# Optimization experiments

Hardware: AMD Instinct MI355X
Metric: run time of the kernel (lower is better)

The kernel has to match this reference:

```python
import jax, jax.numpy as jnp
import numpy as np

N = 100000      # nodes
E = 1600000     # edges (avg degree 16)
IN = 128        # input_dim
H = 8           # heads
D = 8           # hidden_dim (== heads, required by the diversity-loss bmm)
HD = H * D      # per-layer width
OUT = 10        # output_dim
G = 64          # graphs in batch
NEG = 0.2       # GATConv leaky_relu slope
DIVW = 0.1      # diversity_weight


def setup_inputs() -> dict:
    key = jax.random.key(0)
    ks = jax.random.split(key, 20)
    w = lambda k, shape, fan: (jax.random.normal(k, shape, jnp.float32) / np.sqrt(fan)).astype(jnp.float32)
    inp = {}
    inp['x'] = jax.random.normal(ks[0], (N, IN), jnp.float32)
    inp['edge_index'] = jax.random.randint(ks[1], (2, E), 0, N, dtype=jnp.int32)
    inp['batch'] = jnp.sort(jax.random.randint(ks[2], (N,), 0, G, dtype=jnp.int32))
    # layer 0: GATConv(IN -> D, heads=H)
    inp['W0'] = w(ks[3], (IN, HD), IN)
    inp['att_src0'] = w(ks[4], (H, D), D)
    inp['att_dst0'] = w(ks[5], (H, D), D)
    inp['b0'] = jnp.zeros((HD,), jnp.float32)
    inp['gamma0'] = jnp.ones((HD,), jnp.float32)
    inp['beta0'] = jnp.zeros((HD,), jnp.float32)
    inp['P0'] = w(ks[6], (H, D), D)
    # layer 1: GATConv(HD -> D, heads=H)
    inp['W1'] = w(ks[7], (HD, HD), HD)
    inp['att_src1'] = w(ks[8], (H, D), D)
    inp['att_dst1'] = w(ks[9], (H, D), D)
    inp['b1'] = jnp.zeros((HD,), jnp.float32)
    inp['gamma1'] = jnp.ones((HD,), jnp.float32)
    inp['beta1'] = jnp.zeros((HD,), jnp.float32)
    inp['P1'] = w(ks[10], (H, D), D)
    inp['fc_W'] = w(ks[11], (HD, OUT), HD)
    inp['fc_b'] = jnp.zeros((OUT,), jnp.float32)
    return inp


def _gat(x, src, dst, W, a_src, a_dst, b):
    h = (x @ W).reshape(-1, H, D)                       # [N,H,D]
    al = jnp.sum(h * a_src, -1)                          # [N,H] src scores
    ar = jnp.sum(h * a_dst, -1)                          # [N,H] dst scores
    e = jax.nn.leaky_relu(al[src] + ar[dst], NEG)        # [E,H]
    m = jax.ops.segment_max(e, dst, num_segments=N)      # per-dst max (stable softmax)
    m = jnp.where(jnp.isfinite(m), m, 0.0)
    ex = jnp.exp(e - m[dst])
    den = jax.ops.segment_sum(ex, dst, num_segments=N)
    a = ex / (den[dst] + 1e-16)                          # PyG softmax eps
    out = jax.ops.segment_sum(a[:, :, None] * h[src], dst, num_segments=N)  # [N,H,D]
    return out.reshape(-1, HD) + b


def _bn(x, g, b):  # BatchNorm1d, training-mode batch stats, eps=1e-5
    mu = x.mean(0)
    var = x.var(0)
    return g * (x - mu) * jax.lax.rsqrt(var + 1e-5) + b


def _div_loss(x, P):
    xr = x.reshape(-1, H, D)
    pr = jnp.einsum('nij,jk->nik', xr, P)                # bmm with shared projector (needs D==H)
    nh = pr / jnp.maximum(jnp.linalg.norm(pr, axis=-1, keepdims=True), 1e-8)
    S = jnp.einsum('nid,njd->ij', nh, nh) / x.shape[0]   # mean-over-nodes cosine sims [H,H]
    iu = jnp.triu_indices(H, 1)
    return jnp.mean(S[iu] ** 2)


def reference(x, edge_index, batch, W0, att_src0, att_dst0, b0, gamma0, beta0, P0,
              W1, att_src1, att_dst1, b1, gamma1, beta1, P1, fc_W, fc_b):
    src, dst = edge_index[0], edge_index[1]
    dl = 0.0
    h = _gat(x, src, dst, W0, att_src0, att_dst0, b0)
    dl = dl + _div_loss(h, P0)
    h = jax.nn.elu(_bn(h, gamma0, beta0))
    h = _gat(h, src, dst, W1, att_src1, att_dst1, b1)
    dl = dl + _div_loss(h, P1)
    h = jax.nn.elu(_bn(h, gamma1, beta1))
    cnt = jax.ops.segment_sum(jnp.ones((N,), h.dtype), batch, num_segments=G)
    pooled = jax.ops.segment_sum(h, batch, num_segments=G) / jnp.maximum(cnt, 1.0)[:, None]
    logits = pooled @ fc_W + fc_b
    return logits, DIVW * dl
```

## Files before the change

kernel.cpp:

```cpp
#include <hip/hip_runtime.h>
#include <hip/hip_fp16.h>

#define NB 100000
#define NE 1600000
#define PSH 12500
#define BCAP 64

typedef int iv4 __attribute__((ext_vector_type(4)));

__device__ __forceinline__ float elu_f(float x) { return x > 0.f ? x : expm1f(x); }

__global__ __launch_bounds__(256) void k_fill_zero(float4* __restrict__ p, int n4) {
    int i = blockIdx.x * 256 + threadIdx.x, s = gridDim.x * 256;
    float4 z = make_float4(0.f, 0.f, 0.f, 0.f);
    for (; i < n4; i += s) p[i] = z;
}

__global__ __launch_bounds__(256) void k_scatter(const iv4* __restrict__ src4, const iv4* __restrict__ dst4,
                                                 int* __restrict__ cnt, int* __restrict__ buck, int ne4) {
    int part = blockIdx.x & 7;
    unsigned lo = part * PSH;
    int pb = blockIdx.x >> 3, npb = gridDim.x >> 3;
    int i = pb * 256 + threadIdx.x, st = npb * 256;
    for (; i < ne4; i += st) {
        iv4 d = dst4[i];
        bool bx = (unsigned)(d.x - lo) < PSH;
        bool by = (unsigned)(d.y - lo) < PSH;
        bool bz = (unsigned)(d.z - lo) < PSH;
        bool bw = (unsigned)(d.w - lo) < PSH;
        if (!(bx | by | bz | bw)) continue;
        iv4 s = src4[i];
        if (bx) buck[(d.x << 6) + (atomicAdd(&cnt[d.x], 1) & (BCAP - 1))] = s.x;
        if (by) buck[(d.y << 6) + (atomicAdd(&cnt[d.y], 1) & (BCAP - 1))] = s.y;
        if (bz) buck[(d.z << 6) + (atomicAdd(&cnt[d.z], 1) & (BCAP - 1))] = s.z;
        if (bw) buck[(d.w << 6) + (atomicAdd(&cnt[d.w], 1) & (BCAP - 1))] = s.w;
    }
}

template<int K, bool BN>
__global__ __launch_bounds__(256) void k_gemm(
    const float* __restrict__ X, const float* __restrict__ W,
    const float* __restrict__ attS, const float* __restrict__ attD,
    const float* __restrict__ bscale, const float* __restrict__ bshift,
    __half* __restrict__ Hout, float* __restrict__ al, float* __restrict__ ar, int nrows)
{
    constexpr int NC = K / 64;
    __shared__ float4 xs4[64][16];
    __shared__ float  ws_[64][64];
    int t = threadIdx.x;
    int rowBase = blockIdx.x * 64;
    int r = t & 63, cg = t >> 6, c0 = cg * 16;
    float acc[16];
#pragma unroll
    for (int j = 0; j < 16; ++j) acc[j] = 0.f;
    int sw = r & 15;

    for (int kc = 0; kc < NC; ++kc) {
        if (kc) __syncthreads();
        for (int i = t; i < 1024; i += 256)
            ((float4*)ws_)[i] = ((const float4*)W)[kc * 1024 + i];
        for (int i = t; i < 1024; i += 256) {
            int rr = i >> 4, c4 = i & 15;
            int gr = rowBase + rr;
            float4 v = make_float4(0.f, 0.f, 0.f, 0.f);
            if (gr < nrows) v = ((const float4*)X)[gr * (K / 4) + kc * 16 + c4];
            if (BN) {
                int c = (kc * 16 + c4) * 4;
                v.x = elu_f(bscale[c + 0] * v.x + bshift[c + 0]);
                v.y = elu_f(bscale[c + 1] * v.y + bshift[c + 1]);
                v.z = elu_f(bscale[c + 2] * v.z + bshift[c + 2]);
                v.w = elu_f(bscale[c + 3] * v.w + bshift[c + 3]);
            }
            xs4[rr][c4 ^ (rr & 15)] = v;
        }
        __syncthreads();

        for (int k4 = 0; k4 < 16; ++k4) {
            float4 xv = xs4[r][k4 ^ sw];
            float xk[4] = {xv.x, xv.y, xv.z, xv.w};
#pragma unroll
            for (int kk = 0; kk < 4; ++kk) {
                const float* wrow = &ws_[k4 * 4 + kk][c0];
                float4 wa = *(const float4*)(wrow + 0);
                float4 wb = *(const float4*)(wrow + 4);
                float4 wc = *(const float4*)(wrow + 8);
                float4 wd = *(const float4*)(wrow + 12);
                float x = xk[kk];
                acc[0]  += x * wa.x; acc[1]  += x * wa.y; acc[2]  += x * wa.z; acc[3]  += x * wa.w;
                acc[4]  += x * wb.x; acc[5]  += x * wb.y; acc[6]  += x * wb.z; acc[7]  += x * wb.w;
                acc[8]  += x * wc.x; acc[9]  += x * wc.y; acc[10] += x * wc.z; acc[11] += x * wc.w;
                acc[12] += x * wd.x; acc[13] += x * wd.y; acc[14] += x * wd.z; acc[15] += x * wd.w;
            }
        }
    }

    int gr = rowBase + r;
    if (gr < nrows) {
        __half2 hp[8];
#pragma unroll
        for (int j = 0; j < 8; ++j) hp[j] = __floats2half2_rn(acc[2 * j], acc[2 * j + 1]);
        uint4* op = (uint4*)(Hout + (size_t)gr * 64 + c0);
        op[0] = *(uint4*)&hp[0];
        op[1] = *(uint4*)&hp[4];
#pragma unroll
        for (int hh = 0; hh < 2; ++hh) {
            int h = cg * 2 + hh;
            float sa = 0.f, sd = 0.f;
#pragma unroll
            for (int d = 0; d < 8; ++d) {
                float hv = acc[hh * 8 + d];
                sa += hv * attS[h * 8 + d];
                sd += hv * attD[h * 8 + d];
            }
            al[gr * 8 + h] = sa;
            ar[gr * 8 + h] = sd;
        }
    }
}

__global__ __launch_bounds__(256) void k_agg(const int* __restrict__ cnt, const int* __restrict__ buck,
    const float* __restrict__ al, const float* __restrict__ ar,
    const __half* __restrict__ Hf, const float* __restrict__ bias,
    float* __restrict__ agg, int n)
{
    int lane = threadIdx.x & 63;
    int w  = __builtin_amdgcn_readfirstlane((blockIdx.x * 256 + (int)threadIdx.x) >> 6);
    int nw = (gridDim.x * 256) >> 6;
    int h = lane >> 3;
    float bl = bias[lane];
    for (int d = w; d < n; d += nw) {
        int r0 = d << 6;
        int r1 = r0 + __builtin_amdgcn_readfirstlane(cnt[d]);
        float arh = ar[d * 8 + h];
        float ac0 = 0.f, ac1 = 0.f, ac2 = 0.f, ac3 = 0.f, ac4 = 0.f, ac5 = 0.f, ac6 = 0.f, ac7 = 0.f;
        float de0 = 0.f, de1 = 0.f, de2 = 0.f, de3 = 0.f, de4 = 0.f, de5 = 0.f, de6 = 0.f, de7 = 0.f;
        int p = r0;
        for (; p + 8 <= r1; p += 8) {
            int s0 = __builtin_amdgcn_readfirstlane(buck[p]);
            int s1 = __builtin_amdgcn_readfirstlane(buck[p + 1]);
            int s2 = __builtin_amdgcn_readfirstlane(buck[p + 2]);
            int s3 = __builtin_amdgcn_readfirstlane(buck[p + 3]);
            int s4 = __builtin_amdgcn_readfirstlane(buck[p + 4]);
            int s5 = __builtin_amdgcn_readfirstlane(buck[p + 5]);
            int s6 = __builtin_amdgcn_readfirstlane(buck[p + 6]);
            int s7 = __builtin_amdgcn_readfirstlane(buck[p + 7]);
            float t0 = al[s0 * 8 + h] + arh;
            float t1 = al[s1 * 8 + h] + arh;
            float t2 = al[s2 * 8 + h] + arh;
            float t3 = al[s3 * 8 + h] + arh;
            float t4 = al[s4 * 8 + h] + arh;
            float t5 = al[s5 * 8 + h] + arh;
            float t6 = al[s6 * 8 + h] + arh;
            float t7 = al[s7 * 8 + h] + arh;
            float h0 = __half2float(Hf[((size_t)s0 << 6) + lane]);
            float h1 = __half2float(Hf[((size_t)s1 << 6) + lane]);
            float h2 = __half2float(Hf[((size_t)s2 << 6) + lane]);
            float h3 = __half2float(Hf[((size_t)s3 << 6) + lane]);
            float h4 = __half2float(Hf[((size_t)s4 << 6) + lane]);
            float h5 = __half2float(Hf[((size_t)s5 << 6) + lane]);
            float h6 = __half2float(Hf[((size_t)s6 << 6) + lane]);
            float h7 = __half2float(Hf[((size_t)s7 << 6) + lane]);
            t0 = t0 > 0.f ? t0 : 0.2f * t0;  t1 = t1 > 0.f ? t1 : 0.2f * t1;
            t2 = t2 > 0.f ? t2 : 0.2f * t2;  t3 = t3 > 0.f ? t3 : 0.2f * t3;
            t4 = t4 > 0.f ? t4 : 0.2f * t4;  t5 = t5 > 0.f ? t5 : 0.2f * t5;
            t6 = t6 > 0.f ? t6 : 0.2f * t6;  t7 = t7 > 0.f ? t7 : 0.2f * t7;
            float e0 = __expf(t0), e1 = __expf(t1), e2 = __expf(t2), e3 = __expf(t3);
            float e4 = __expf(t4), e5 = __expf(t5), e6 = __expf(t6), e7 = __expf(t7);
            de0 += e0; ac0 = fmaf(e0, h0, ac0);
            de1 += e1; ac1 = fmaf(e1, h1, ac1);
            de2 += e2; ac2 = fmaf(e2, h2, ac2);
            de3 += e3; ac3 = fmaf(e3, h3, ac3);
            de4 += e4; ac4 = fmaf(e4, h4, ac4);
            de5 += e5; ac5 = fmaf(e5, h5, ac5);
            de6 += e6; ac6 = fmaf(e6, h6, ac6);
            de7 += e7; ac7 = fmaf(e7, h7, ac7);
        }
        for (; p + 4 <= r1; p += 4) {
            int s0 = __builtin_amdgcn_readfirstlane(buck[p]);
            int s1 = __builtin_amdgcn_readfirstlane(buck[p + 1]);
            int s2 = __builtin_amdgcn_readfirstlane(buck[p + 2]);
            int s3 = __builtin_amdgcn_readfirstlane(buck[p + 3]);
            float t0 = al[s0 * 8 + h] + arh;
            float t1 = al[s1 * 8 + h] + arh;
            float t2 = al[s2 * 8 + h] + arh;
            float t3 = al[s3 * 8 + h] + arh;
            float h0 = __half2float(Hf[((size_t)s0 << 6) + lane]);
            float h1 = __half2float(Hf[((size_t)s1 << 6) + lane]);
            float h2 = __half2float(Hf[((size_t)s2 << 6) + lane]);
            float h3 = __half2float(Hf[((size_t)s3 << 6) + lane]);
            t0 = t0 > 0.f ? t0 : 0.2f * t0;  t1 = t1 > 0.f ? t1 : 0.2f * t1;
            t2 = t2 > 0.f ? t2 : 0.2f * t2;  t3 = t3 > 0.f ? t3 : 0.2f * t3;
            float e0 = __expf(t0), e1 = __expf(t1), e2 = __expf(t2), e3 = __expf(t3);
            de0 += e0; ac0 = fmaf(e0, h0, ac0);
            de1 += e1; ac1 = fmaf(e1, h1, ac1);
            de2 += e2; ac2 = fmaf(e2, h2, ac2);
            de3 += e3; ac3 = fmaf(e3, h3, ac3);
        }
        for (; p < r1; ++p) {
            int s0 = __builtin_amdgcn_readfirstlane(buck[p]);
            float t0 = al[s0 * 8 + h] + arh;
            float h0 = __half2float(Hf[((size_t)s0 << 6) + lane]);
            t0 = t0 > 0.f ? t0 : 0.2f * t0;
            float e0 = __expf(t0);
            de0 += e0; ac0 = fmaf(e0, h0, ac0);
        }
        float den = ((de0 + de1) + (de2 + de3)) + ((de4 + de5) + (de6 + de7));
        float num = ((ac0 + ac1) + (ac2 + ac3)) + ((ac4 + ac5) + (ac6 + ac7));
        float inv = 1.f / (den + 1e-16f);
        agg[(size_t)d * 64 + lane] = fmaf(num, inv, bl);
    }
}

__global__ __launch_bounds__(256) void k_post(const float* __restrict__ agg, const float* __restrict__ P,
    float* __restrict__ Sord, float* __restrict__ bsum, float* __restrict__ bsq, int n)
{
    __shared__ float Ps[64];
    __shared__ float red[4][184];
    int t = threadIdx.x;
    if (t < 64) Ps[t] = P[t];
    __syncthreads();
    int lane = t & 63, wid = t >> 6;
    int h = lane & 7, grp = lane >> 3;
    int w  = (blockIdx.x * 256 + t) >> 6;
    int nw = (gridDim.x * 256) >> 6;
    float sacc[7], bs[8], bq[8];
#pragma unroll
    for (int i = 0; i < 7; ++i) sacc[i] = 0.f;
#pragma unroll
    for (int i = 0; i < 8; ++i) { bs[i] = 0.f; bq[i] = 0.f; }

    for (int base = w * 8; base < n; base += nw * 8) {
        int node = base + grp;
        float xv[8];
        if (node < n) {
            const float4* rp = (const float4*)(agg + (size_t)node * 64 + h * 8);
            float4 a = rp[0], b = rp[1];
            xv[0]=a.x; xv[1]=a.y; xv[2]=a.z; xv[3]=a.w; xv[4]=b.x; xv[5]=b.y; xv[6]=b.z; xv[7]=b.w;
        } else {
#pragma unroll
            for (int k = 0; k < 8; ++k) xv[k] = 0.f;
        }
#pragma unroll
        for (int k = 0; k < 8; ++k) { bs[k] += xv[k]; bq[k] += xv[k] * xv[k]; }
        float pr[8];
#pragma unroll
        for (int k = 0; k < 8; ++k) pr[k] = 0.f;
#pragma unroll
        for (int j = 0; j < 8; ++j) {
            float x = xv[j];
#pragma unroll
            for (int k = 0; k < 8; ++k) pr[k] += x * Ps[j * 8 + k];
        }
        float nrm2 = 0.f;
#pragma unroll
        for (int k = 0; k < 8; ++k) nrm2 += pr[k] * pr[k];
        float inv = 1.f / fmaxf(sqrtf(nrm2), 1e-8f);
#pragma unroll
        for (int k = 0; k < 8; ++k) pr[k] *= inv;
#pragma unroll
        for (int d = 1; d < 8; ++d) {
            float dot = 0.f;
#pragma unroll
            for (int k = 0; k < 8; ++k) dot += pr[k] * __shfl_xor(pr[k], d, 64);
            sacc[d - 1] += dot;
        }
    }
#pragma unroll
    for (int d = 0; d < 7; ++d) {
        sacc[d] += __shfl_xor(sacc[d], 8, 64);
        sacc[d] += __shfl_xor(sacc[d], 16, 64);
        sacc[d] += __shfl_xor(sacc[d], 32, 64);
    }
#pragma unroll
    for (int k = 0; k < 8; ++k) {
        bs[k] += __shfl_xor(bs[k], 8, 64); bs[k] += __shfl_xor(bs[k], 16, 64); bs[k] += __shfl_xor(bs[k], 32, 64);
        bq[k] += __shfl_xor(bq[k], 8, 64); bq[k] += __shfl_xor(bq[k], 16, 64); bq[k] += __shfl_xor(bq[k], 32, 64);
    }
    if (lane < 8) {
#pragma unroll
        for (int d = 0; d < 7; ++d) red[wid][h * 23 + d] = sacc[d];
#pragma unroll
        for (int k = 0; k < 8; ++k) { red[wid][h * 23 + 7 + k] = bs[k]; red[wid][h * 23 + 15 + k] = bq[k]; }
    }
    __syncthreads();
    if (t < 184) {
        float v = red[0][t] + red[1][t] + red[2][t] + red[3][t];
        int hh = t / 23, r = t % 23;
        if (r < 7)       atomicAdd(&Sord[hh * 8 + (hh ^ (r + 1))], v);
        else if (r < 15) atomicAdd(&bsum[hh * 8 + (r - 7)], v);
        else             atomicAdd(&bsq [hh * 8 + (r - 15)], v);
    }
}

__global__ void k_bn_fin(const float* __restrict__ sum, const float* __restrict__ sumsq,
                         const float* __restrict__ gamma, const float* __restrict__ beta,
                         float* __restrict__ scale, float* __restrict__ shift, int n)
{
    int c = threadIdx.x;
    float invn = 1.f / (float)n;
    float mu = sum[c] * invn;
    float var = sumsq[c] * invn - mu * mu;
    float sc = gamma[c] * rsqrtf(var + 1e-5f);
    scale[c] = sc;
    shift[c] = beta[c] - mu * sc;
}

__global__ __launch_bounds__(256) void k_pool(const float* __restrict__ agg, const int* __restrict__ batch,
    const float* __restrict__ scale, const float* __restrict__ shift,
    float* __restrict__ psum, float* __restrict__ cnt, int n)
{
    int lane = threadIdx.x & 63;
    int w  = (blockIdx.x * 256 + threadIdx.x) >> 6;
    int nw = (gridDim.x * 256) >> 6;
    int chunk = (n + nw - 1) / nw;
    int n0 = w * chunk;
    if (n0 >= n) return;
    int n1 = min(n, n0 + chunk);
    float sc = scale[lane], sh = shift[lane];
    float acc = 0.f;
    int curg = batch[n0], run = 0;
    for (int i = n0; i < n1; ++i) {
        int g = batch[i];
        if (g != curg) {
            atomicAdd(psum + curg * 64 + lane, acc);
            if (lane == 0) atomicAdd(cnt + curg, (float)run);
            acc = 0.f; run = 0; curg = g;
        }
        float v = agg[(size_t)i * 64 + lane];
        v = sc * v + sh;
        v = v > 0.f ? v : expm1f(v);
        acc += v; run += 1;
    }
    atomicAdd(psum + curg * 64 + lane, acc);
    if (lane == 0) atomicAdd(cnt + curg, (float)run);
}

__global__ __launch_bounds__(640) void k_final(const float* __restrict__ psum, const float* __restrict__ cnt,
    const float* __restrict__ fcW, const float* __restrict__ fcb,
    const float* __restrict__ S0, const float* __restrict__ S1,
    float* __restrict__ out, int n)
{
    __shared__ float pl[64][65];
    int t = threadIdx.x;
    for (int i = t; i < 4096; i += 640) {
        int g = i >> 6, c = i & 63;
        pl[g][c] = psum[i] / fmaxf(cnt[g], 1.f);
    }
    __syncthreads();
    {
        int g = t / 10, o = t % 10;
        float s = fcb[o];
#pragma unroll 8
        for (int c = 0; c < 64; ++c) s += pl[g][c] * fcW[c * 10 + o];
        out[g * 10 + o] = s;
    }
    if (t == 0) {
        float invn = 1.f / (float)n;
        float dl = 0.f;
        for (int i = 0; i < 8; ++i)
            for (int j = i + 1; j < 8; ++j) {
                float v0 = S0[i * 8 + j] * invn; dl += v0 * v0;
                float v1 = S1[i * 8 + j] * invn; dl += v1 * v1;
            }
        out[640] = 0.1f * (dl / 28.f);
    }
}

extern "C" void kernel_launch(void* const* d_in, const int* in_sizes, int n_in,
                              void* d_out, int out_size, void* d_ws, size_t ws_size,
                              hipStream_t stream)
{
    const float* x   = (const float*)d_in[0];
    const int*   ei  = (const int*)d_in[1];
    const int*   bat = (const int*)d_in[2];
    const float* W0  = (const float*)d_in[3];
    const float* as0 = (const float*)d_in[4];
    const float* ad0 = (const float*)d_in[5];
    const float* b0  = (const float*)d_in[6];
    const float* g0  = (const float*)d_in[7];
    const float* be0 = (const float*)d_in[8];
    const float* P0  = (const float*)d_in[9];
    const float* W1  = (const float*)d_in[10];
    const float* as1 = (const float*)d_in[11];
    const float* ad1 = (const float*)d_in[12];
    const float* b1  = (const float*)d_in[13];
    const float* g1  = (const float*)d_in[14];
    const float* be1 = (const float*)d_in[15];
    const float* P1  = (const float*)d_in[16];
    const float* fcW = (const float*)d_in[17];
    const float* fcb = (const float*)d_in[18];
    const int* src = ei;
    const int* dst = ei + NE;

    float* ws    = (float*)d_ws;
    __half* Hbuf = (__half*)ws;
    float* agg   = ws + 6400000;
    float* al    = ws + 12800000;
    float* ar    = ws + 13600000;
    float* stats = ws + 14400000;
    float* psum  = ws + 14401024;
    int*   cnt   = (int*)(ws + 14405120);
    int*   buck  = cnt + NB;

    float* Sord0 = stats + 0;
    float* Sord1 = stats + 64;
    float* sum0  = stats + 128;
    float* sq0   = stats + 192;
    float* sum1  = stats + 256;
    float* sq1   = stats + 320;
    float* sc0   = stats + 384;
    float* sh0   = stats + 448;
    float* sc1   = stats + 512;
    float* sh1   = stats + 576;
    float* gcnt  = stats + 640;

    k_fill_zero<<<103, 256, 0, stream>>>((float4*)stats, 26280);

    k_scatter<<<2048, 256, 0, stream>>>((const iv4*)src, (const iv4*)dst, cnt, buck, NE / 4);

    k_gemm<128, false><<<1563, 256, 0, stream>>>(x, W0, as0, ad0, nullptr, nullptr, Hbuf, al, ar, NB);
    k_agg<<<25000, 256, 0, stream>>>(cnt, buck, al, ar, Hbuf, b0, agg, NB);
    k_post<<<512, 256, 0, stream>>>(agg, P0, Sord0, sum0, sq0, NB);
    k_bn_fin<<<1, 64, 0, stream>>>(sum0, sq0, g0, be0, sc0, sh0, NB);

    k_gemm<64, true><<<1563, 256, 0, stream>>>(agg, W1, as1, ad1, sc0, sh0, Hbuf, al, ar, NB);
    k_agg<<<25000, 256, 0, stream>>>(cnt, buck, al, ar, Hbuf, b1, agg, NB);
    k_post<<<512, 256, 0, stream>>>(agg, P1, Sord1, sum1, sq1, NB);
    k_bn_fin<<<1, 64, 0, stream>>>(sum1, sq1, g1, be1, sc1, sh1, NB);

    k_pool<<<512, 256, 0, stream>>>(agg, bat, sc1, sh1, psum, gcnt, NB);
    k_final<<<1, 640, 0, stream>>>(psum, gcnt, fcW, fcb, Sord0, Sord1, (float*)d_out, NB);
}
```

Baseline: 368.7 us.

## Co-schedule edge scatter with layer-0 GEMM and fold BN finalize into consumers

Merges the edge bucketing scatter and the first GEMM into one launch whose blocks are interleaved, so the atomic-heavy scatter overlaps with compute-bound GEMM work. Removes the two single-block BN finalize kernels and recomputes scale and shift inside the layer-1 GEMM (cached in shared memory) and the pooling kernel. This cuts launch count and serialization gaps, at the cost of some redundant per-block BN arithmetic and a more complex block-role mapping.

```diff
diff --git a/kernel.cpp b/kernel.cpp
--- a/kernel.cpp
+++ b/kernel.cpp
@@ -5,6 +5,9 @@
 #define NE 1600000
 #define PSH 12500
 #define BCAP 64
+#define SCB 2048
+#define GMB 1568
+#define MIXB 3136
 
 typedef int iv4 __attribute__((ext_vector_type(4)));
 
@@ -16,46 +19,55 @@
     for (; i < n4; i += s) p[i] = z;
 }
 
-__global__ __launch_bounds__(256) void k_scatter(const iv4* __restrict__ src4, const iv4* __restrict__ dst4,
-                                                 int* __restrict__ cnt, int* __restrict__ buck, int ne4) {
-    int part = blockIdx.x & 7;
-    unsigned lo = part * PSH;
-    int pb = blockIdx.x >> 3, npb = gridDim.x >> 3;
-    int i = pb * 256 + threadIdx.x, st = npb * 256;
-    for (; i < ne4; i += st) {
-        iv4 d = dst4[i];
-        bool bx = (unsigned)(d.x - lo) < PSH;
-        bool by = (unsigned)(d.y - lo) < PSH;
-        bool bz = (unsigned)(d.z - lo) < PSH;
-        bool bw = (unsigned)(d.w - lo) < PSH;
-        if (!(bx | by | bz | bw)) continue;
-        iv4 s = src4[i];
-        if (bx) buck[(d.x << 6) + (atomicAdd(&cnt[d.x], 1) & (BCAP - 1))] = s.x;
-        if (by) buck[(d.y << 6) + (atomicAdd(&cnt[d.y], 1) & (BCAP - 1))] = s.y;
-        if (bz) buck[(d.z << 6) + (atomicAdd(&cnt[d.z], 1) & (BCAP - 1))] = s.z;
-        if (bw) buck[(d.w << 6) + (atomicAdd(&cnt[d.w], 1) & (BCAP - 1))] = s.w;
-    }
-}
-
-template<int K, bool BN>
-__global__ __launch_bounds__(256) void k_gemm(
+__global__ __launch_bounds__(256) void k_scat_gemm(
+    const iv4* __restrict__ src4, const iv4* __restrict__ dst4,
+    int* __restrict__ cnt, int* __restrict__ buck, int ne4,
     const float* __restrict__ X, const float* __restrict__ W,
     const float* __restrict__ attS, const float* __restrict__ attD,
-    const float* __restrict__ bscale, const float* __restrict__ bshift,
     __half* __restrict__ Hout, float* __restrict__ al, float* __restrict__ ar, int nrows)
 {
-    constexpr int NC = K / 64;
     __shared__ float4 xs4[64][16];
     __shared__ float  ws_[64][64];
-    int t = threadIdx.x;
-    int rowBase = blockIdx.x * 64;
+    int b = blockIdx.x, t = threadIdx.x;
+    int isS, idx;
+    if (b < MIXB) {
+        int g = b >> 3;
+        isS = g & 1;
+        idx = (g >> 1) * 8 + (b & 7);
+    } else {
+        isS = 1;
+        idx = GMB + (b - MIXB);
+    }
+
+    if (isS) {
+        int part = idx & 7;
+        unsigned lo = part * PSH;
+        int pb = idx >> 3;
+        int i = pb * 256 + t, st = (SCB >> 3) * 256;
+        for (; i < ne4; i += st) {
+            iv4 d = dst4[i];
+            bool bx = (unsigned)(d.x - lo) < PSH;
+            bool by = (unsigned)(d.y - lo) < PSH;
+            bool bz = (unsigned)(d.z - lo) < PSH;
+            bool bw = (unsigned)(d.w - lo) < PSH;
+            if (!(bx | by | bz | bw)) continue;
+            iv4 s = src4[i];
+            if (bx) buck[(d.x << 6) + (atomicAdd(&cnt[d.x], 1) & (BCAP - 1))] = s.x;
+            if (by) buck[(d.y << 6) + (atomicAdd(&cnt[d.y], 1) & (BCAP - 1))] = s.y;
+            if (bz) buck[(d.z << 6) + (atomicAdd(&cnt[d.z], 1) & (BCAP - 1))] = s.z;
+            if (bw) buck[(d.w << 6) + (atomicAdd(&cnt[d.w], 1) & (BCAP - 1))] = s.w;
+        }
+        return;
+    }
+
+    int rowBase = idx * 64;
     int r = t & 63, cg = t >> 6, c0 = cg * 16;
     float acc[16];
 #pragma unroll
     for (int j = 0; j < 16; ++j) acc[j] = 0.f;
     int sw = r & 15;
 
-    for (int kc = 0; kc < NC; ++kc) {
+    for (int kc = 0; kc < 2; ++kc) {
         if (kc) __syncthreads();
         for (int i = t; i < 1024; i += 256)
             ((float4*)ws_)[i] = ((const float4*)W)[kc * 1024 + i];
@@ -63,18 +75,10 @@
             int rr = i >> 4, c4 = i & 15;
             int gr = rowBase + rr;
             float4 v = make_float4(0.f, 0.f, 0.f, 0.f);
-            if (gr < nrows) v = ((const float4*)X)[gr * (K / 4) + kc * 16 + c4];
-            if (BN) {
-                int c = (kc * 16 + c4) * 4;
-                v.x = elu_f(bscale[c + 0] * v.x + bshift[c + 0]);
-                v.y = elu_f(bscale[c + 1] * v.y + bshift[c + 1]);
-                v.z = elu_f(bscale[c + 2] * v.z + bshift[c + 2]);
-                v.w = elu_f(bscale[c + 3] * v.w + bshift[c + 3]);
-            }
+            if (gr < nrows) v = ((const float4*)X)[gr * 32 + kc * 16 + c4];
             xs4[rr][c4 ^ (rr & 15)] = v;
         }
         __syncthreads();
-
         for (int k4 = 0; k4 < 16; ++k4) {
             float4 xv = xs4[r][k4 ^ sw];
             float xk[4] = {xv.x, xv.y, xv.z, xv.w};
@@ -104,6 +108,90 @@
         op[1] = *(uint4*)&hp[4];
 #pragma unroll
         for (int hh = 0; hh < 2; ++hh) {
+            int h = cg * 2 + hh;
+            float sa = 0.f, sd = 0.f;
+#pragma unroll
+            for (int d = 0; d < 8; ++d) {
+                float hv = acc[hh * 8 + d];
+                sa += hv * attS[h * 8 + d];
+                sd += hv * attD[h * 8 + d];
+            }
+            al[gr * 8 + h] = sa;
+            ar[gr * 8 + h] = sd;
+        }
+    }
+}
+
+__global__ __launch_bounds__(256) void k_gemm1(
+    const float* __restrict__ X, const float* __restrict__ W,
+    const float* __restrict__ attS, const float* __restrict__ attD,
+    const float* __restrict__ bsum, const float* __restrict__ bsq,
+    const float* __restrict__ gamma, const float* __restrict__ beta,
+    __half* __restrict__ Hout, float* __restrict__ al, float* __restrict__ ar, int nrows)
+{
+    __shared__ float4 xs4[64][16];
+    __shared__ float  ws_[64][64];
+    __shared__ float  sc_[64], sh_[64];
+    int t = threadIdx.x;
+    int rowBase = blockIdx.x * 64;
+    if (t < 64) {
+        float invn = 1.f / (float)NB;
+        float mu = bsum[t] * invn;
+        float var = bsq[t] * invn - mu * mu;
+        float s = gamma[t] * rsqrtf(var + 1e-5f);
+        sc_[t] = s;
+        sh_[t] = beta[t] - mu * s;
+    }
+    for (int i = t; i < 1024; i += 256)
+        ((float4*)ws_)[i] = ((const float4*)W)[i];
+    __syncthreads();
+
+    for (int i = t; i < 1024; i += 256) {
+        int rr = i >> 4, c4 = i & 15;
+        int gr = rowBase + rr;
+        float4 v = make_float4(0.f, 0.f, 0.f, 0.f);
+        if (gr < nrows) v = ((const float4*)X)[gr * 16 + c4];
+        int c = c4 * 4;
+        v.x = elu_f(sc_[c + 0] * v.x + sh_[c + 0]);
+        v.y = elu_f(sc_[c + 1] * v.y + sh_[c + 1]);
+        v.z = elu_f(sc_[c + 2] * v.z + sh_[c + 2]);
+        v.w = elu_f(sc_[c + 3] * v.w + sh_[c + 3]);
+        xs4[rr][c4 ^ (rr & 15)] = v;
+    }
+    __syncthreads();
+
+    int r = t & 63, cg = t >> 6, c0 = cg * 16;
+    float acc[16];
+#pragma unroll
+    for (int j = 0; j < 16; ++j) acc[j] = 0.f;
+    int sw = r & 15;
+    for (int k4 = 0; k4 < 16; ++k4) {
+        float4 xv = xs4[r][k4 ^ sw];
+        float xk[4] = {xv.x, xv.y, xv.z, xv.w};
+#pragma unroll
+        for (int kk = 0; kk < 4; ++kk) {
+            const float* wrow = &ws_[k4 * 4 + kk][c0];
+            float4 wa = *(const float4*)(wrow + 0);
+            float4 wb = *(const float4*)(wrow + 4);
+            float4 wc = *(const float4*)(wrow + 8);
+            float4 wd = *(const float4*)(wrow + 12);
+            float x = xk[kk];
+            acc[0]  += x * wa.x; acc[1]  += x * wa.y; acc[2]  += x * wa.z; acc[3]  += x * wa.w;
+            acc[4]  += x * wb.x; acc[5]  += x * wb.y; acc[6]  += x * wb.z; acc[7]  += x * wb.w;
+            acc[8]  += x * wc.x; acc[9]  += x * wc.y; acc[10] += x * wc.z; acc[11] += x * wc.w;
+            acc[12] += x * wd.x; acc[13] += x * wd.y; acc[14] += x * wd.z; acc[15] += x * wd.w;
+        }
+    }
+    int gr = rowBase + r;
+    if (gr < nrows) {
+        __half2 hp[8];
+#pragma unroll
+        for (int j = 0; j < 8; ++j) hp[j] = __floats2half2_rn(acc[2 * j], acc[2 * j + 1]);
+        uint4* op = (uint4*)(Hout + (size_t)gr * 64 + c0);
+        op[0] = *(uint4*)&hp[0];
+        op[1] = *(uint4*)&hp[4];
+#pragma unroll
+    for (int hh = 0; hh < 2; ++hh) {
             int h = cg * 2 + hh;
             float sa = 0.f, sd = 0.f;
 #pragma unroll
@@ -292,21 +380,9 @@
     }
 }
 
-__global__ void k_bn_fin(const float* __restrict__ sum, const float* __restrict__ sumsq,
-                         const float* __restrict__ gamma, const float* __restrict__ beta,
-                         float* __restrict__ scale, float* __restrict__ shift, int n)
-{
-    int c = threadIdx.x;
-    float invn = 1.f / (float)n;
-    float mu = sum[c] * invn;
-    float var = sumsq[c] * invn - mu * mu;
-    float sc = gamma[c] * rsqrtf(var + 1e-5f);
-    scale[c] = sc;
-    shift[c] = beta[c] - mu * sc;
-}
-
 __global__ __launch_bounds__(256) void k_pool(const float* __restrict__ agg, const int* __restrict__ batch,
-    const float* __restrict__ scale, const float* __restrict__ shift,
+    const float* __restrict__ bsum, const float* __restrict__ bsq,
+    const float* __restrict__ gamma, const float* __restrict__ beta,
     float* __restrict__ psum, float* __restrict__ cnt, int n)
 {
     int lane = threadIdx.x & 63;
@@ -316,7 +392,11 @@
     int n0 = w * chunk;
     if (n0 >= n) return;
     int n1 = min(n, n0 + chunk);
-    float sc = scale[lane], sh = shift[lane];
+    float invn = 1.f / (float)n;
+    float mu = bsum[lane] * invn;
+    float var = bsq[lane] * invn - mu * mu;
+    float sc = gamma[lane] * rsqrtf(var + 1e-5f);
+    float sh = beta[lane] - mu * sc;
     float acc = 0.f;
     int curg = batch[n0], run = 0;
     for (int i = n0; i < n1; ++i) {
@@ -408,26 +488,20 @@
     float* sq0   = stats + 192;
     float* sum1  = stats + 256;
     float* sq1   = stats + 320;
-    float* sc0   = stats + 384;
-    float* sh0   = stats + 448;
-    float* sc1   = stats + 512;
-    float* sh1   = stats + 576;
     float* gcnt  = stats + 640;
 
     k_fill_zero<<<103, 256, 0, stream>>>((float4*)stats, 26280);
 
-    k_scatter<<<2048, 256, 0, stream>>>((const iv4*)src, (const iv4*)dst, cnt, buck, NE / 4);
-
-    k_gemm<128, false><<<1563, 256, 0, stream>>>(x, W0, as0, ad0, nullptr, nullptr, Hbuf, al, ar, NB);
+    k_scat_gemm<<<SCB + GMB, 256, 0, stream>>>((const iv4*)src, (const iv4*)dst, cnt, buck, NE / 4,
+                                               x, W0, as0, ad0, Hbuf, al, ar, NB);
+
     k_agg<<<25000, 256, 0, stream>>>(cnt, buck, al, ar, Hbuf, b0, agg, NB);
     k_post<<<512, 256, 0, stream>>>(agg, P0, Sord0, sum0, sq0, NB);
-    k_bn_fin<<<1, 64, 0, stream>>>(sum0, sq0, g0, be0, sc0, sh0, NB);
-
-    k_gemm<64, true><<<1563, 256, 0, stream>>>(agg, W1, as1, ad1, sc0, sh0, Hbuf, al, ar, NB);
+
+    k_gemm1<<<1563, 256, 0, stream>>>(agg, W1, as1, ad1, sum0, sq0, g0, be0, Hbuf, al, ar, NB);
     k_agg<<<25000, 256, 0, stream>>>(cnt, buck, al, ar, Hbuf, b1, agg, NB);
     k_post<<<512, 256, 0, stream>>>(agg, P1, Sord1, sum1, sq1, NB);
-    k_bn_fin<<<1, 64, 0, stream>>>(sum1, sq1, g1, be1, sc1, sh1, NB);
-
-    k_pool<<<512, 256, 0, stream>>>(agg, bat, sc1, sh1, psum, gcnt, NB);
+
+    k_pool<<<512, 256, 0, stream>>>(agg, bat, sum1, sq1, g1, be1, psum, gcnt, NB);
     k_final<<<1, 640, 0, stream>>>(psum, gcnt, fcW, fcb, Sord0, Sord1, (float*)d_out, NB);
 }
```

After: 327.6 us. 1.13x faster.
